# Kernel tuning notes

Hardware: AMD Instinct MI355X
Metric: run time of the kernel (lower is better)

Reference implementation:

```python
import jax, jax.numpy as jnp
import numpy as np

B = 16384      # batch
N = 128        # number of DNPU nodes (experts)
I = 3          # data electrodes per node
C = 4          # control electrodes per node
E = I + C      # total electrodes = 7
H = 90         # surrogate-model hidden width
L = 3          # number of extra hidden layers


def setup_inputs() -> dict:
    key = jax.random.key(0)
    ks = jax.random.split(key, 8)
    s_in = 1.0 / np.sqrt(E)
    s_h = 1.0 / np.sqrt(H)
    return {
        "x": jax.random.normal(ks[0], (B, N * I), dtype=jnp.float32),
        "controls": jax.random.uniform(ks[1], (N, C), dtype=jnp.float32, minval=-1.2, maxval=0.6),
        "W_in": jax.random.normal(ks[2], (N, E, H), dtype=jnp.float32) * s_in,
        "b_in": jax.random.normal(ks[3], (N, H), dtype=jnp.float32) * 0.1,
        "W_hid": jax.random.normal(ks[4], (L, N, H, H), dtype=jnp.float32) * s_h,
        "b_hid": jax.random.normal(ks[5], (L, N, H), dtype=jnp.float32) * 0.1,
        "W_out": jax.random.normal(ks[6], (N, H), dtype=jnp.float32) * s_h,
        "b_out": jax.random.normal(ks[7], (N,), dtype=jnp.float32) * 0.1,
    }


def reference(x, controls, W_in, b_in, W_hid, b_hid, W_out, b_out):
    # DNPU_Layer: partition x into N chunks of I, each node merges its data
    # electrodes with its learned control voltages into a 7-electrode vector,
    # evaluates the shared surrogate MLP with per-node parameters, outputs 1
    # current per node; results are concatenated along dim 1 -> [B, N].
    b = x.shape[0]
    xd = x.reshape(b, N, I)                                   # partition_input
    ctrl = jnp.broadcast_to(controls[None], (b, N, C))        # per-node controls
    e = jnp.concatenate([xd, ctrl], axis=-1)                  # [B, N, E]
    h = jax.nn.relu(jnp.einsum('bne,neh->bnh', e, W_in) + b_in)
    for l in range(L):  # fixed small layer count
        h = jax.nn.relu(jnp.einsum('bnh,nhk->bnk', h, W_hid[l]) + b_hid[l])
    out = jnp.einsum('bnh,nh->bn', h, W_out) + b_out          # [B, N]
    return out
```

## Files before the change

kernel.cpp:

```cpp
#include <hip/hip_runtime.h>
#include <stdint.h>

namespace {
constexpr int kB  = 16384;
constexpr int kN  = 128;
constexpr int kI  = 3;
constexpr int kC  = 4;
constexpr int kH  = 90;
constexpr int kL  = 3;
constexpr int BT  = 64;
constexpr int KP  = 96;
constexpr int TILE_USH = 18 * 512;
constexpr size_t WT_BYTES = (size_t)4 * kN * TILE_USH * 2;
constexpr size_t WO_OFF   = WT_BYTES;
constexpr size_t XK_OFF   = WO_OFF + (size_t)kN * KP * 4;
constexpr size_t OT_OFF   = XK_OFF + (size_t)kN * kI * kB * 2;
}

typedef __attribute__((ext_vector_type(8))) short bf16x8;
typedef __attribute__((ext_vector_type(4))) float f32x4;

__device__ __forceinline__ uint32_t pack_bf16(float lo, float hi) {
#if __has_builtin(__builtin_amdgcn_cvt_pk_bf16_f32)
  auto r = __builtin_amdgcn_cvt_pk_bf16_f32(lo, hi);
  union { decltype(r) v; uint32_t u; } c; c.v = r; return c.u;
#else
  union { float f; uint32_t i; } a, b; a.f = lo; b.f = hi;
  uint32_t ua = a.i + 0x8000u;
  uint32_t ub = b.i + 0x8000u;
  return __builtin_amdgcn_perm(ub, ua, 0x07060302);
#endif
}
__device__ __forceinline__ ushort f2bf(float f) {
  union { float f; uint32_t i; } v; v.f = f;
  uint32_t u = v.i + 0x7FFFu + ((v.i >> 16) & 1u);
  return (ushort)(u >> 16);
}

__global__ __launch_bounds__(256) void prep_kernel(
    const float* __restrict__ x,
    const float* __restrict__ W_in, const float* __restrict__ b_in,
    const float* __restrict__ W_hid, const float* __restrict__ b_hid,
    const float* __restrict__ W_out, const float* __restrict__ b_out,
    ushort* __restrict__ wt, float* __restrict__ wo, ushort* __restrict__ xk)
{
  __shared__ float smem[kH * (kH + 1) + kH];
  const int tid = threadIdx.x;
  const int bid = blockIdx.x;

  if (bid < 4 * kN) {
    float* ldsw = smem;
    float* ldsb = smem + kH * (kH + 1);
    const int node  = bid & (kN - 1);
    const int layer = bid >> 7;
    const int ksrc  = (layer == 0) ? (kI + kC) : kH;
    const float* src;
    const float* bsrc;
    if (layer == 0) { src = W_in + (size_t)node * (kI + kC) * kH; bsrc = b_in + (size_t)node * kH; }
    else {
      int l = layer - 1;
      src  = W_hid + (size_t)(l * kN + node) * kH * kH;
      bsrc = b_hid + (size_t)(l * kN + node) * kH;
    }
    for (int idx = tid; idx < ksrc * kH; idx += 256)
      ldsw[(idx / kH) * (kH + 1) + (idx % kH)] = src[idx];
    if (tid < kH) ldsb[tid] = bsrc[tid];
    __syncthreads();
    ushort* dst = wt + (size_t)bid * TILE_USH;
    const int nch = (layer == 0) ? 384 : 1152;
#pragma unroll
    for (int it = 0; it < 5; ++it) {
      int c = tid + it * 256;
      if (c < nch) {
        int fb = c >> 6, lane = c & 63;
        int mt = fb % 6, ks = fb / 6;
        int j = mt * 16 + (lane & 15);
        int kb = ks * 32 + (lane >> 4) * 8;
        float v[8];
#pragma unroll
        for (int i = 0; i < 8; ++i) {
          int k = kb + i;
          float t = 0.f;
          if (j < kH) {
            if (k < ksrc)       t = ldsw[k * (kH + 1) + j];
            else if (k == ksrc) t = ldsb[j];
          }
          v[i] = t;
        }
        uint4 p;
        p.x = pack_bf16(v[0], v[1]); p.y = pack_bf16(v[2], v[3]);
        p.z = pack_bf16(v[4], v[5]); p.w = pack_bf16(v[6], v[7]);
        *(uint4*)&dst[(size_t)c * 8] = p;
      }
    }
  } else if (bid < 4 * kN + 4) {
    int base = (bid - 4 * kN) * 3072;
    for (int t = 0; t < 12; ++t) {
      int idx = base + t * 256 + tid;
      int node = idx / KP, j = idx % KP;
      float v = 0.f;
      if (j < kH)       v = W_out[node * kH + j];
      else if (j == kH) v = b_out[node];
      wo[idx] = v;
    }
  } else {
    int xb = bid - (4 * kN + 4);
    int b0 = (xb & 255) * 64;
    int c0 = (xb >> 8) * 96;
    float* lds = smem;
    for (int idx = tid; idx < 64 * 96; idx += 256) {
      int r = idx / 96, c = idx % 96;
      lds[r * 97 + c] = x[(size_t)(b0 + r) * (kN * kI) + c0 + c];
    }
    __syncthreads();
#pragma unroll
    for (int it = 0; it < 3; ++it) {
      int c = tid + it * 256;
      int nk = c >> 3, b = (c & 7) * 8;
      float v[8];
#pragma unroll
      for (int i = 0; i < 8; ++i) v[i] = lds[(b + i) * 97 + nk];
      uint4 p;
      p.x = pack_bf16(v[0], v[1]); p.y = pack_bf16(v[2], v[3]);
      p.z = pack_bf16(v[4], v[5]); p.w = pack_bf16(v[6], v[7]);
      *(uint4*)&xk[(size_t)(c0 + nk) * kB + b0 + b] = p;
    }
  }
}

__global__ __launch_bounds__(64, 3) void dnpu_kernel(
    const ushort* __restrict__ xk, const float* __restrict__ controls,
    const ushort* __restrict__ wt, const float* __restrict__ wo,
    float* __restrict__ outT)
{
  __shared__ __align__(16) ushort fbuf[12][BT][8];

  const int lane = threadIdx.x;
  const int node = (int)(blockIdx.x & 127);
  const int m0   = (int)(blockIdx.x >> 7) * BT;
  const int quad = lane >> 4;
  const int l16  = lane & 15;

  const f32x4 zf = (f32x4){0.f, 0.f, 0.f, 0.f};
  f32x4 acc[6][4];

  bf16x8 bfr0[4];
  {
    const ushort cb0 = f2bf(controls[node * kC + 0]);
    const ushort cb1 = f2bf(controls[node * kC + 1]);
    const ushort cb2 = f2bf(controls[node * kC + 2]);
    const ushort cb3 = f2bf(controls[node * kC + 3]);
    if (quad == 0) {
      const ushort* x0p = xk + (size_t)(node * kI + 0) * kB + m0 + l16;
      const ushort* x1p = xk + (size_t)(node * kI + 1) * kB + m0 + l16;
      const ushort* x2p = xk + (size_t)(node * kI + 2) * kB + m0 + l16;
#pragma unroll
      for (int nt = 0; nt < 4; ++nt) {
        union { ushort s[8]; bf16x8 v; } f;
        f.s[0] = x0p[nt * 16]; f.s[1] = x1p[nt * 16]; f.s[2] = x2p[nt * 16];
        f.s[3] = cb0; f.s[4] = cb1; f.s[5] = cb2; f.s[6] = cb3;
        f.s[7] = 0x3F80;
        bfr0[nt] = f.v;
      }
    } else {
#pragma unroll
      for (int nt = 0; nt < 4; ++nt)
        bfr0[nt] = (bf16x8){0,0,0,0,0,0,0,0};
    }
  }

  {
    const ushort* tl = wt + (size_t)(0 * kN + node) * TILE_USH;
#pragma unroll
    for (int mt = 0; mt < 6; ++mt) {
      bf16x8 afr = *(const bf16x8*)&tl[(size_t)mt * 512 + lane * 8];
#pragma unroll
      for (int nt = 0; nt < 4; ++nt)
        acc[mt][nt] = __builtin_amdgcn_mfma_f32_16x16x32_bf16(afr, bfr0[nt], zf, 0, 0, 0);
    }
  }

  auto write_h = [&]() {
#pragma unroll
    for (int mt = 0; mt < 6; ++mt) {
      const int kb = 2 * mt + (quad >> 1);
      const int i0 = (quad & 1) * 4;
#pragma unroll
      for (int nt = 0; nt < 4; ++nt) {
        float v0 = fmaxf(acc[mt][nt][0], 0.f);
        float v1 = fmaxf(acc[mt][nt][1], 0.f);
        float v2 = fmaxf(acc[mt][nt][2], 0.f);
        float v3 = fmaxf(acc[mt][nt][3], 0.f);
        if (mt == 5 && quad == 2) v2 = 1.0f;
        uint2 p;
        p.x = pack_bf16(v0, v1);
        p.y = pack_bf16(v2, v3);
        *(uint2*)&fbuf[kb][nt * 16 + l16][i0] = p;
      }
    }
  };

#pragma unroll
  for (int l = 0; l < kL; ++l) {
    const ushort* tl = wt + (size_t)((l + 1) * kN + node) * TILE_USH;
    write_h();

    {
      bf16x8 bfr[4];
#pragma unroll
      for (int nt = 0; nt < 4; ++nt)
        bfr[nt] = *(const bf16x8*)&fbuf[quad][nt * 16 + l16][0];
#pragma unroll
      for (int mt = 0; mt < 6; ++mt) {
        bf16x8 afr = *(const bf16x8*)&tl[(size_t)mt * 512 + lane * 8];
#pragma unroll
        for (int nt = 0; nt < 4; ++nt)
          acc[mt][nt] = __builtin_amdgcn_mfma_f32_16x16x32_bf16(afr, bfr[nt], zf, 0, 0, 0);
      }
    }
#pragma unroll
    for (int ks = 1; ks < 3; ++ks) {
      bf16x8 bfr[4];
#pragma unroll
      for (int nt = 0; nt < 4; ++nt)
        bfr[nt] = *(const bf16x8*)&fbuf[ks * 4 + quad][nt * 16 + l16][0];
#pragma unroll
      for (int mt = 0; mt < 6; ++mt) {
        bf16x8 afr = *(const bf16x8*)&tl[(size_t)(ks * 6 + mt) * 512 + lane * 8];
#pragma unroll
        for (int nt = 0; nt < 4; ++nt)
          acc[mt][nt] = __builtin_amdgcn_mfma_f32_16x16x32_bf16(afr, bfr[nt], acc[mt][nt], 0, 0, 0);
      }
    }
  }

  {
    float4 wof[6];
#pragma unroll
    for (int mt = 0; mt < 6; ++mt)
      wof[mt] = *(const float4*)&wo[node * KP + mt * 16 + quad * 4];
    float s[4] = {0.f, 0.f, 0.f, 0.f};
#pragma unroll
    for (int mt = 0; mt < 6; ++mt) {
#pragma unroll
      for (int nt = 0; nt < 4; ++nt) {
        float h0 = fmaxf(acc[mt][nt][0], 0.f);
        float h1 = fmaxf(acc[mt][nt][1], 0.f);
        float h2 = fmaxf(acc[mt][nt][2], 0.f);
        float h3 = fmaxf(acc[mt][nt][3], 0.f);
        if (mt == 5 && quad == 2) h2 = 1.0f;
        s[nt] += h0 * wof[mt].x + h1 * wof[mt].y + h2 * wof[mt].z + h3 * wof[mt].w;
      }
    }
#pragma unroll
    for (int nt = 0; nt < 4; ++nt) {
      s[nt] += __shfl_xor(s[nt], 16);
      s[nt] += __shfl_xor(s[nt], 32);
    }
    float r = (quad == 0) ? s[0] : (quad == 1) ? s[1] : (quad == 2) ? s[2] : s[3];
    outT[(size_t)node * kB + m0 + lane] = r;
  }
}

__global__ __launch_bounds__(256) void transpose_out(
    const float* __restrict__ ot, float* __restrict__ out)
{
  __shared__ float t[64][65];
  const int b0 = (int)(blockIdx.x & 255) * 64;
  const int n0 = (int)(blockIdx.x >> 8) * 64;
  const int c  = threadIdx.x & 63;
  const int r4 = threadIdx.x >> 6;
#pragma unroll
  for (int i = 0; i < 16; ++i) {
    int n = r4 + i * 4;
    t[n][c] = ot[(size_t)(n0 + n) * kB + b0 + c];
  }
  __syncthreads();
#pragma unroll
  for (int i = 0; i < 16; ++i) {
    int b = r4 + i * 4;
    out[(size_t)(b0 + b) * kN + n0 + c] = t[c][b];
  }
}

extern "C" void kernel_launch(void* const* d_in, const int* in_sizes, int n_in,
                              void* d_out, int out_size, void* d_ws, size_t ws_size,
                              hipStream_t stream) {
  const float* x        = (const float*)d_in[0];
  const float* controls = (const float*)d_in[1];
  const float* W_in     = (const float*)d_in[2];
  const float* b_in     = (const float*)d_in[3];
  const float* W_hid    = (const float*)d_in[4];
  const float* b_hid    = (const float*)d_in[5];
  const float* W_out    = (const float*)d_in[6];
  const float* b_out    = (const float*)d_in[7];
  float* out = (float*)d_out;

  ushort* wt = (ushort*)d_ws;
  float*  wo = (float*)((char*)d_ws + WO_OFF);
  ushort* xk = (ushort*)((char*)d_ws + XK_OFF);
  float*  ot = (float*)((char*)d_ws + OT_OFF);

  hipLaunchKernelGGL(prep_kernel, dim3(4 * kN + 4 + 1024), dim3(256), 0, stream,
                     x, W_in, b_in, W_hid, b_hid, W_out, b_out, wt, wo, xk);

  dim3 grid((kB / BT) * kN);
  hipLaunchKernelGGL(dnpu_kernel, grid, dim3(64), 0, stream,
                     xk, controls, wt, wo, ot);

  hipLaunchKernelGGL(transpose_out, dim3(512), dim3(256), 0, stream, ot, out);
}
```

Baseline: 228.5 us.

## Switch to 32x32x16 MFMA with register-resident activations via permlane32 swap

Replaces the 16x16x32 bf16 MFMA tiling with 32x32x16 MFMA tiles and repacks the weight layout per node to match. The hidden activations are no longer staged through LDS. They are rearranged between accumulator and B-operand layout in registers using permlane32_swap. The aim is to remove LDS round-trips and use the larger MFMA shape. The trade-off is more register pressure from the 16-wide accumulators and the packed B fragments, which could hurt occupancy.

```diff
diff --git a/kernel.cpp b/kernel.cpp
--- a/kernel.cpp
+++ b/kernel.cpp
@@ -10,8 +10,9 @@
 constexpr int kL  = 3;
 constexpr int BT  = 64;
 constexpr int KP  = 96;
-constexpr int TILE_USH = 18 * 512;
-constexpr size_t WT_BYTES = (size_t)4 * kN * TILE_USH * 2;
+constexpr int FB_PER_NODE = 57;
+constexpr int NODE_USH    = FB_PER_NODE * 512;
+constexpr size_t WT_BYTES = (size_t)kN * NODE_USH * 2;
 constexpr size_t WO_OFF   = WT_BYTES;
 constexpr size_t XK_OFF   = WO_OFF + (size_t)kN * KP * 4;
 constexpr size_t OT_OFF   = XK_OFF + (size_t)kN * kI * kB * 2;
@@ -19,6 +20,7 @@
 
 typedef __attribute__((ext_vector_type(8))) short bf16x8;
 typedef __attribute__((ext_vector_type(4))) float f32x4;
+typedef __attribute__((ext_vector_type(16))) float f32x16;
 
 __device__ __forceinline__ uint32_t pack_bf16(float lo, float hi) {
 #if __has_builtin(__builtin_amdgcn_cvt_pk_bf16_f32)
@@ -35,6 +37,20 @@
   union { float f; uint32_t i; } v; v.f = f;
   uint32_t u = v.i + 0x7FFFu + ((v.i >> 16) & 1u);
   return (ushort)(u >> 16);
+}
+
+__device__ __forceinline__ void pl32swap(uint32_t& a, uint32_t& b) {
+#if __has_builtin(__builtin_amdgcn_permlane32_swap)
+  auto r = __builtin_amdgcn_permlane32_swap(a, b, false, false);
+  a = (uint32_t)r[0]; b = (uint32_t)r[1];
+#else
+  uint32_t sa = (uint32_t)__shfl_xor((int)a, 32);
+  uint32_t sb = (uint32_t)__shfl_xor((int)b, 32);
+  bool lo = (threadIdx.x & 63) < 32;
+  uint32_t na = lo ? a : sb;
+  uint32_t nb = lo ? sa : b;
+  a = na; b = nb;
+#endif
 }
 
 __global__ __launch_bounds__(256) void prep_kernel(
@@ -66,16 +82,18 @@
       ldsw[(idx / kH) * (kH + 1) + (idx % kH)] = src[idx];
     if (tid < kH) ldsb[tid] = bsrc[tid];
     __syncthreads();
-    ushort* dst = wt + (size_t)bid * TILE_USH;
-    const int nch = (layer == 0) ? 384 : 1152;
+    ushort* dstbase = wt + (size_t)node * NODE_USH
+                    + (size_t)((layer == 0) ? 0 : 3 + (layer - 1) * 18) * 512;
+    const int nch = (layer == 0) ? 192 : 1152;
 #pragma unroll
     for (int it = 0; it < 5; ++it) {
       int c = tid + it * 256;
       if (c < nch) {
         int fb = c >> 6, lane = c & 63;
-        int mt = fb % 6, ks = fb / 6;
-        int j = mt * 16 + (lane & 15);
-        int kb = ks * 32 + (lane >> 4) * 8;
+        int ks = (layer == 0) ? 0 : fb / 3;
+        int mt = (layer == 0) ? fb : fb % 3;
+        int j  = mt * 32 + (lane & 31);
+        int kb = ks * 16 + (lane >> 5) * 8;
         float v[8];
 #pragma unroll
         for (int i = 0; i < 8; ++i) {
@@ -90,7 +108,7 @@
         uint4 p;
         p.x = pack_bf16(v[0], v[1]); p.y = pack_bf16(v[2], v[3]);
         p.z = pack_bf16(v[4], v[5]); p.w = pack_bf16(v[6], v[7]);
-        *(uint4*)&dst[(size_t)c * 8] = p;
+        *(uint4*)&dstbase[(size_t)c * 8] = p;
       }
     }
   } else if (bid < 4 * kN + 4) {
@@ -133,131 +151,113 @@
     const ushort* __restrict__ wt, const float* __restrict__ wo,
     float* __restrict__ outT)
 {
-  __shared__ __align__(16) ushort fbuf[12][BT][8];
-
   const int lane = threadIdx.x;
   const int node = (int)(blockIdx.x & 127);
   const int m0   = (int)(blockIdx.x >> 7) * BT;
-  const int quad = lane >> 4;
-  const int l16  = lane & 15;
-
-  const f32x4 zf = (f32x4){0.f, 0.f, 0.f, 0.f};
-  f32x4 acc[6][4];
-
-  bf16x8 bfr0[4];
+  const int col  = lane & 31;
+  const int hh   = lane >> 5;
+
+  const f32x16 zf = (f32x16)0.0f;
+  f32x16 acc[3][2];
+
+  bf16x8 b0[2];
   {
     const ushort cb0 = f2bf(controls[node * kC + 0]);
     const ushort cb1 = f2bf(controls[node * kC + 1]);
     const ushort cb2 = f2bf(controls[node * kC + 2]);
     const ushort cb3 = f2bf(controls[node * kC + 3]);
-    if (quad == 0) {
-      const ushort* x0p = xk + (size_t)(node * kI + 0) * kB + m0 + l16;
-      const ushort* x1p = xk + (size_t)(node * kI + 1) * kB + m0 + l16;
-      const ushort* x2p = xk + (size_t)(node * kI + 2) * kB + m0 + l16;
-#pragma unroll
-      for (int nt = 0; nt < 4; ++nt) {
-        union { ushort s[8]; bf16x8 v; } f;
-        f.s[0] = x0p[nt * 16]; f.s[1] = x1p[nt * 16]; f.s[2] = x2p[nt * 16];
-        f.s[3] = cb0; f.s[4] = cb1; f.s[5] = cb2; f.s[6] = cb3;
-        f.s[7] = 0x3F80;
-        bfr0[nt] = f.v;
+    const ushort* xp = xk + (size_t)node * kI * kB + m0 + col;
+#pragma unroll
+    for (int nt = 0; nt < 2; ++nt) {
+      union { ushort s[8]; bf16x8 v; } f;
+      f.s[0] = xp[0 * kB + nt * 32];
+      f.s[1] = xp[1 * kB + nt * 32];
+      f.s[2] = xp[2 * kB + nt * 32];
+      f.s[3] = cb0; f.s[4] = cb1; f.s[5] = cb2; f.s[6] = cb3;
+      f.s[7] = 0x3F80;
+      bf16x8 z = (bf16x8){0,0,0,0,0,0,0,0};
+      if (hh) b0[nt] = z; else b0[nt] = f.v;
+    }
+  }
+
+  {
+    const ushort* t0 = wt + (size_t)node * NODE_USH;
+#pragma unroll
+    for (int mt = 0; mt < 3; ++mt) {
+      bf16x8 afr = *(const bf16x8*)&t0[mt * 512 + lane * 8];
+#pragma unroll
+      for (int nt = 0; nt < 2; ++nt)
+        acc[mt][nt] = __builtin_amdgcn_mfma_f32_32x32x16_bf16(afr, b0[nt], zf, 0, 0, 0);
+    }
+  }
+
+  union BF { uint32_t u[4]; bf16x8 v; };
+  BF Bw[6][2];
+
+  auto packB = [&]() {
+#pragma unroll
+    for (int mt = 0; mt < 3; ++mt)
+#pragma unroll
+      for (int nt = 0; nt < 2; ++nt) {
+        float v[16];
+#pragma unroll
+        for (int r = 0; r < 16; ++r) v[r] = fmaxf(acc[mt][nt][r], 0.f);
+        if (mt == 2) v[14] = (hh == 0) ? 1.0f : v[14];
+        uint32_t P[8];
+#pragma unroll
+        for (int w = 0; w < 8; ++w) P[w] = pack_bf16(v[2 * w], v[2 * w + 1]);
+        uint32_t a0 = P[0], c0 = P[2]; pl32swap(a0, c0);
+        uint32_t a1 = P[1], c1 = P[3]; pl32swap(a1, c1);
+        uint32_t a2 = P[4], c2 = P[6]; pl32swap(a2, c2);
+        uint32_t a3 = P[5], c3 = P[7]; pl32swap(a3, c3);
+        Bw[2 * mt][nt].u[0] = a0; Bw[2 * mt][nt].u[1] = a1;
+        Bw[2 * mt][nt].u[2] = c0; Bw[2 * mt][nt].u[3] = c1;
+        Bw[2 * mt + 1][nt].u[0] = a2; Bw[2 * mt + 1][nt].u[1] = a3;
+        Bw[2 * mt + 1][nt].u[2] = c2; Bw[2 * mt + 1][nt].u[3] = c3;
       }
-    } else {
-#pragma unroll
-      for (int nt = 0; nt < 4; ++nt)
-        bfr0[nt] = (bf16x8){0,0,0,0,0,0,0,0};
-    }
+  };
+
+#pragma unroll
+  for (int l = 0; l < kL; ++l) {
+    packB();
+    const ushort* tl = wt + (size_t)node * NODE_USH + (size_t)(3 + l * 18) * 512;
+#pragma unroll
+    for (int ks = 0; ks < 6; ++ks)
+#pragma unroll
+      for (int mt = 0; mt < 3; ++mt) {
+        bf16x8 afr = *(const bf16x8*)&tl[(size_t)(ks * 3 + mt) * 512 + lane * 8];
+#pragma unroll
+        for (int nt = 0; nt < 2; ++nt)
+          acc[mt][nt] = __builtin_amdgcn_mfma_f32_32x32x16_bf16(
+              afr, Bw[ks][nt].v, (ks == 0) ? zf : acc[mt][nt], 0, 0, 0);
+      }
   }
 
   {
-    const ushort* tl = wt + (size_t)(0 * kN + node) * TILE_USH;
-#pragma unroll
-    for (int mt = 0; mt < 6; ++mt) {
-      bf16x8 afr = *(const bf16x8*)&tl[(size_t)mt * 512 + lane * 8];
-#pragma unroll
-      for (int nt = 0; nt < 4; ++nt)
-        acc[mt][nt] = __builtin_amdgcn_mfma_f32_16x16x32_bf16(afr, bfr0[nt], zf, 0, 0, 0);
-    }
-  }
-
-  auto write_h = [&]() {
-#pragma unroll
-    for (int mt = 0; mt < 6; ++mt) {
-      const int kb = 2 * mt + (quad >> 1);
-      const int i0 = (quad & 1) * 4;
-#pragma unroll
-      for (int nt = 0; nt < 4; ++nt) {
-        float v0 = fmaxf(acc[mt][nt][0], 0.f);
-        float v1 = fmaxf(acc[mt][nt][1], 0.f);
-        float v2 = fmaxf(acc[mt][nt][2], 0.f);
-        float v3 = fmaxf(acc[mt][nt][3], 0.f);
-        if (mt == 5 && quad == 2) v2 = 1.0f;
-        uint2 p;
-        p.x = pack_bf16(v0, v1);
-        p.y = pack_bf16(v2, v3);
-        *(uint2*)&fbuf[kb][nt * 16 + l16][i0] = p;
+    const float* wop = wo + node * KP;
+    float s0 = 0.f, s1 = 0.f;
+#pragma unroll
+    for (int mt = 0; mt < 3; ++mt) {
+#pragma unroll
+      for (int g = 0; g < 4; ++g) {
+        float4 wf = *(const float4*)&wop[mt * 32 + g * 8 + hh * 4];
+#pragma unroll
+        for (int r2 = 0; r2 < 4; ++r2) {
+          int r = g * 4 + r2;
+          float w = (r2 == 0) ? wf.x : (r2 == 1) ? wf.y : (r2 == 2) ? wf.z : wf.w;
+          float h0v = fmaxf(acc[mt][0][r], 0.f);
+          float h1v = fmaxf(acc[mt][1][r], 0.f);
+          if (mt == 2 && r == 14) {
+            h0v = (hh == 0) ? 1.0f : h0v;
+            h1v = (hh == 0) ? 1.0f : h1v;
+          }
+          s0 += h0v * w; s1 += h1v * w;
+        }
       }
     }
-  };
-
-#pragma unroll
-  for (int l = 0; l < kL; ++l) {
-    const ushort* tl = wt + (size_t)((l + 1) * kN + node) * TILE_USH;
-    write_h();
-
-    {
-      bf16x8 bfr[4];
-#pragma unroll
-      for (int nt = 0; nt < 4; ++nt)
-        bfr[nt] = *(const bf16x8*)&fbuf[quad][nt * 16 + l16][0];
-#pragma unroll
-      for (int mt = 0; mt < 6; ++mt) {
-        bf16x8 afr = *(const bf16x8*)&tl[(size_t)mt * 512 + lane * 8];
-#pragma unroll
-        for (int nt = 0; nt < 4; ++nt)
-          acc[mt][nt] = __builtin_amdgcn_mfma_f32_16x16x32_bf16(afr, bfr[nt], zf, 0, 0, 0);
-      }
-    }
-#pragma unroll
-    for (int ks = 1; ks < 3; ++ks) {
-      bf16x8 bfr[4];
-#pragma unroll
-      for (int nt = 0; nt < 4; ++nt)
-        bfr[nt] = *(const bf16x8*)&fbuf[ks * 4 + quad][nt * 16 + l16][0];
-#pragma unroll
-      for (int mt = 0; mt < 6; ++mt) {
-        bf16x8 afr = *(const bf16x8*)&tl[(size_t)(ks * 6 + mt) * 512 + lane * 8];
-#pragma unroll
-        for (int nt = 0; nt < 4; ++nt)
-          acc[mt][nt] = __builtin_amdgcn_mfma_f32_16x16x32_bf16(afr, bfr[nt], acc[mt][nt], 0, 0, 0);
-      }
-    }
-  }
-
-  {
-    float4 wof[6];
-#pragma unroll
-    for (int mt = 0; mt < 6; ++mt)
-      wof[mt] = *(const float4*)&wo[node * KP + mt * 16 + quad * 4];
-    float s[4] = {0.f, 0.f, 0.f, 0.f};
-#pragma unroll
-    for (int mt = 0; mt < 6; ++mt) {
-#pragma unroll
-      for (int nt = 0; nt < 4; ++nt) {
-        float h0 = fmaxf(acc[mt][nt][0], 0.f);
-        float h1 = fmaxf(acc[mt][nt][1], 0.f);
-        float h2 = fmaxf(acc[mt][nt][2], 0.f);
-        float h3 = fmaxf(acc[mt][nt][3], 0.f);
-        if (mt == 5 && quad == 2) h2 = 1.0f;
-        s[nt] += h0 * wof[mt].x + h1 * wof[mt].y + h2 * wof[mt].z + h3 * wof[mt].w;
-      }
-    }
-#pragma unroll
-    for (int nt = 0; nt < 4; ++nt) {
-      s[nt] += __shfl_xor(s[nt], 16);
-      s[nt] += __shfl_xor(s[nt], 32);
-    }
-    float r = (quad == 0) ? s[0] : (quad == 1) ? s[1] : (quad == 2) ? s[2] : s[3];
+    s0 += __shfl_xor(s0, 32);
+    s1 += __shfl_xor(s1, 32);
+    float r = hh ? s1 : s0;
     outT[(size_t)node * kB + m0 + lane] = r;
   }
 }
```

Result: slower. 244.3 us (+6.9%).
